# Performance work log

Hardware: AMD Instinct MI355X
Metric: run time of the kernel (lower is better)

## Reference

```python
import jax, jax.numpy as jnp
import numpy as np

B, T, N, D = 32, 50, 100, 4
E = N * (N - 1)
N_IN, N_HID, N_OUT = T * D, 256, 4


def _mlp(x, w1, b1, w2, b2):
    # Linear -> ReLU -> (dropout=0) -> Linear
    return jax.nn.relu(x @ w1 + b1) @ w2 + b2


def setup_inputs() -> dict:
    key = jax.random.key(0)
    ks = jax.random.split(key, 12)
    # fully-connected directed graph, no self loops
    idx = np.array([(i, j) for i in range(N) for j in range(N) if i != j], dtype=np.int64)
    recv, sendr = idx[:, 0], idx[:, 1]
    rec = jnp.asarray(np.eye(N, dtype=np.float32)[recv])    # [E, N]
    send = jnp.asarray(np.eye(N, dtype=np.float32)[sendr])  # [E, N]

    def lin(k, fan_in, fan_out):
        kw, kb = jax.random.split(k)
        w = jax.random.normal(kw, (fan_in, fan_out), jnp.float32) * 0.02
        b = jax.random.normal(kb, (fan_out,), jnp.float32) * 0.02
        return w, b

    x = jax.random.normal(ks[0], (B, T, N, D), jnp.float32)
    w1a, b1a = lin(ks[1], N_IN, N_HID)
    w1b, b1b = lin(ks[2], N_HID, N_HID)
    w2a, b2a = lin(ks[3], 2 * N_HID, N_HID)
    w2b, b2b = lin(ks[4], N_HID, N_HID)
    w3a, b3a = lin(ks[5], N_HID, N_HID)
    w3b, b3b = lin(ks[6], N_HID, N_HID)
    w4a, b4a = lin(ks[7], 3 * N_HID, N_HID)
    w4b, b4b = lin(ks[8], N_HID, N_HID)
    wo, bo = lin(ks[9], N_HID, N_OUT)
    return {"x": x, "rec": rec, "send": send,
            "w1a": w1a, "b1a": b1a, "w1b": w1b, "b1b": b1b,
            "w2a": w2a, "b2a": b2a, "w2b": w2b, "b2b": b2b,
            "w3a": w3a, "b3a": b3a, "w3b": w3b, "b3b": b3b,
            "w4a": w4a, "b4a": b4a, "w4b": w4b, "b4b": b4b,
            "wo": wo, "bo": bo}


def reference(x, rec, send,
              w1a, b1a, w1b, b1b,
              w2a, b2a, w2b, b2b,
              w3a, b3a, w3b, b3b,
              w4a, b4a, w4b, b4b,
              wo, bo):
    # [B, T, N, D] -> [B, N, T*D]
    h = jnp.transpose(x, (0, 2, 1, 3)).reshape(x.shape[0], x.shape[2], -1)
    h = _mlp(h, w1a, b1a, w1b, b1b)                       # [B, N, H]
    # v2e: gather receiver/sender node states to edges
    e = jnp.concatenate([jnp.einsum('en,bnh->beh', rec, h),
                         jnp.einsum('en,bnh->beh', send, h)], axis=2)  # [B, E, 2H]
    e = _mlp(e, w2a, b2a, w2b, b2b)                       # [B, E, H]
    x_skip = e
    # e2v: scatter edges back to nodes, normalize by n_nodes
    v = jnp.einsum('en,beh->bnh', rec, e) / e.shape[-2] * (e.shape[-2] / rec.shape[1])
    v = jnp.einsum('en,beh->bnh', rec, e) / rec.shape[1]  # incoming / incoming.size(1)=N
    v = _mlp(v, w3a, b3a, w3b, b3b)                       # [B, N, H]
    e2 = jnp.concatenate([jnp.einsum('en,bnh->beh', rec, v),
                          jnp.einsum('en,bnh->beh', send, v)], axis=2)  # [B, E, 2H]
    e2 = jnp.concatenate([e2, x_skip], axis=2)            # [B, E, 3H]
    e2 = _mlp(e2, w4a, b4a, w4b, b4b)                     # [B, E, H]
    return e2 @ wo + bo                                   # [B, E, n_out]
```

## Files before the change

### kernel.cpp

```cpp
#include <hip/hip_runtime.h>
#include <hip/hip_bf16.h>
#include <stdint.h>


typedef __attribute__((ext_vector_type(8))) short short8;
typedef __attribute__((ext_vector_type(4))) float float4v;
typedef __attribute__((ext_vector_type(4))) unsigned short ushort4v;
typedef __attribute__((ext_vector_type(4))) unsigned int uint4v;
typedef __attribute__((ext_vector_type(2))) unsigned int uint2v;

__device__ inline float bf2f(unsigned short u) {
    union { unsigned int i; float f; } v; v.i = ((unsigned int)u) << 16; return v.f;
}

#if __has_builtin(__builtin_amdgcn_cvt_pk_bf16_f32)
typedef __attribute__((ext_vector_type(2))) __bf16 bf16x2;
__device__ inline unsigned int f2bf_pk(float a, float b) {
    union { bf16x2 v; unsigned int u; } c;
    c.v = __builtin_amdgcn_cvt_pk_bf16_f32(a, b);
    return c.u;
}
__device__ inline unsigned short f2bf(float f) {
    return (unsigned short)(f2bf_pk(f, f) & 0xFFFFu);
}
#else
__device__ inline unsigned short f2bf(float f) {
    union { float f; unsigned int i; } v; v.f = f;
    unsigned int i = v.i;
    return (unsigned short)((i + 0x7FFFu + ((i >> 16) & 1u)) >> 16);
}
__device__ inline unsigned int f2bf_pk(float a, float b) {
    return (unsigned int)f2bf(a) | ((unsigned int)f2bf(b) << 16);
}
#endif

__global__ __launch_bounds__(256) void prep_kernel(
        const float* __restrict__ x,
        const float* __restrict__ w1a, const float* __restrict__ w1b,
        const float* __restrict__ w2a, const float* __restrict__ w2b,
        const float* __restrict__ w3a, const float* __restrict__ w3b,
        const float* __restrict__ w4a, const float* __restrict__ b4a,
        const float* __restrict__ w4b, const float* __restrict__ b4b,
        const float* __restrict__ wo,  const float* __restrict__ bo,
        const float* __restrict__ b2b,
        unsigned short* __restrict__ Wp1a, unsigned short* __restrict__ Wp1b,
        unsigned short* __restrict__ Wp2r, unsigned short* __restrict__ Wp2s,
        unsigned short* __restrict__ Wp2b, unsigned short* __restrict__ Wp3a,
        unsigned short* __restrict__ Wp3b, unsigned short* __restrict__ Wp4r,
        unsigned short* __restrict__ Wp4s, unsigned short* __restrict__ Wpz,
        unsigned short* __restrict__ Wfp, float* __restrict__ bfv,
        float* __restrict__ b4ap, float* __restrict__ b2bs,
        unsigned short* __restrict__ hin) {
    int bx = blockIdx.x;
    int tid = threadIdx.x;
    if (bx < 2272) {
        const float* W; unsigned short* Wp; int Kin; int b0;
        if      (bx <  224) { W = w1a;             Wp = Wp1a; Kin = 200; b0 = 0;    }
        else if (bx <  480) { W = w1b;             Wp = Wp1b; Kin = 256; b0 = 224;  }
        else if (bx <  736) { W = w2a;             Wp = Wp2r; Kin = 256; b0 = 480;  }
        else if (bx <  992) { W = w2a + 256 * 256; Wp = Wp2s; Kin = 256; b0 = 736;  }
        else if (bx < 1248) { W = w2b;             Wp = Wp2b; Kin = 256; b0 = 992;  }
        else if (bx < 1504) { W = w3a;             Wp = Wp3a; Kin = 256; b0 = 1248; }
        else if (bx < 1760) { W = w3b;             Wp = Wp3b; Kin = 256; b0 = 1504; }
        else if (bx < 2016) { W = w4a;             Wp = Wp4r; Kin = 256; b0 = 1760; }
        else                { W = w4a + 256 * 256; Wp = Wp4s; Kin = 256; b0 = 2016; }
        int idx = (bx - b0) * 256 + tid;
        int k = idx >> 8, n = idx & 255;
        unsigned short v = (k < Kin) ? f2bf(W[k * 256 + n]) : (unsigned short)0;
        Wp[((size_t)(k >> 5) * 256 + n) * 32 + (k & 31)] = v;
    } else if (bx < 2528) {
        int k = bx - 2272, c = tid;
        float s = 0.f;
        for (int t = 0; t < 256; ++t)
            s += w2b[k * 256 + t] * w4a[(size_t)(512 + t) * 256 + c];
        int n = (c & ~31) + (c & 1) * 16 + ((c & 31) >> 1);
        Wpz[((size_t)(k >> 5) * 256 + n) * 32 + (k & 31)] = f2bf(s);
    } else if (bx < 2530) {
        int k = tid;
        if (bx == 2528) {
            float a[4] = {0.f, 0.f, 0.f, 0.f};
            for (int c = 0; c < 256; ++c) {
                float wv = w4b[k * 256 + c];
                #pragma unroll
                for (int o = 0; o < 4; ++o) a[o] += wv * wo[c * 4 + o];
            }
            #pragma unroll
            for (int n = 0; n < 16; ++n)
                Wfp[(size_t)(k >> 5) * 512 + n * 32 + (k & 31)] =
                    (n < 4) ? f2bf(a[n]) : (unsigned short)0;
            if (k < 4) {
                float s = bo[k];
                for (int c = 0; c < 256; ++c) s += b4b[c] * wo[c * 4 + k];
                bfv[k] = s;
            }
        } else {
            float s = b4a[k];
            for (int t = 0; t < 256; ++t)
                s += b2b[t] * w4a[(size_t)(512 + t) * 256 + k];
            b4ap[k] = s;
            b2bs[k] = 0.99f * b2b[k];
        }
    } else {
        int idx = (bx - 2530) * 256 + tid;
        if (idx < 3200 * 224) {
            int row = idx / 224;
            int c = idx - row * 224;
            int b = row / 100, n = row - b * 100;
            unsigned short v = 0;
            if (c < 200) {
                int t = c >> 2, d = c & 3;
                v = f2bf(x[(((size_t)(b * 50 + t)) * 100 + n) * 4 + d]);
            }
            hin[(size_t)row * 224 + c] = v;
        }
    }
}

__global__ __launch_bounds__(512) void node_fusedA_kernel(
        const unsigned short* __restrict__ hin,
        const unsigned short* __restrict__ Wp1a, const float* __restrict__ b1a,
        const unsigned short* __restrict__ Wp1b, const float* __restrict__ b1b,
        const unsigned short* __restrict__ Wp2r, const float* __restrict__ b2a,
        const unsigned short* __restrict__ Wp2s,
        unsigned short* __restrict__ U, unsigned short* __restrict__ Hs) {
    __shared__ __align__(16) unsigned short t1s[16 * 264];
    __shared__ __align__(16) unsigned short hs2[16 * 264];
    const int m0 = blockIdx.x * 16;
    const int tid  = threadIdx.x;
    const int wave = tid >> 6;
    const int lane = tid & 63;
    const int l15  = lane & 15;
    const int quad = lane >> 4;
    const int n0   = wave * 32;
    const int koff = quad * 8;

    {
        float4v acc[2];
        acc[0] = (float4v)(0.0f); acc[1] = (float4v)(0.0f);
        for (int kb = 0; kb < 7; ++kb) {
            short8 af = *(const short8*)(hin + (size_t)(m0 + l15) * 224 + kb * 32 + koff);
            #pragma unroll
            for (int ni = 0; ni < 2; ++ni) {
                short8 bf = *(const short8*)(Wp1a + ((size_t)kb * 256 + n0 + ni * 16 + l15) * 32 + koff);
                acc[ni] = __builtin_amdgcn_mfma_f32_16x16x32_bf16(af, bf, acc[ni], 0, 0, 0);
            }
        }
        #pragma unroll
        for (int ni = 0; ni < 2; ++ni) {
            int col = n0 + ni * 16 + l15;
            float bv = b1a[col];
            #pragma unroll
            for (int r = 0; r < 4; ++r) {
                float v = acc[ni][r] + bv;
                v = v > 0.f ? v : 0.f;
                t1s[(quad * 4 + r) * 264 + col] = f2bf(v);
            }
        }
    }
    __syncthreads();

    {
        float4v acc[2];
        acc[0] = (float4v)(0.0f); acc[1] = (float4v)(0.0f);
        for (int kb = 0; kb < 8; ++kb) {
            short8 af = *(const short8*)(&t1s[l15 * 264 + kb * 32 + koff]);
            #pragma unroll
            for (int ni = 0; ni < 2; ++ni) {
                short8 bf = *(const short8*)(Wp1b + ((size_t)kb * 256 + n0 + ni * 16 + l15) * 32 + koff);
                acc[ni] = __builtin_amdgcn_mfma_f32_16x16x32_bf16(af, bf, acc[ni], 0, 0, 0);
            }
        }
        #pragma unroll
        for (int ni = 0; ni < 2; ++ni) {
            int col = n0 + ni * 16 + l15;
            float bv = b1b[col];
            #pragma unroll
            for (int r = 0; r < 4; ++r)
                hs2[(quad * 4 + r) * 264 + col] = f2bf(acc[ni][r] + bv);
        }
    }
    __syncthreads();

    {
        float4v aU[2], aH[2];
        aU[0] = (float4v)(0.0f); aU[1] = (float4v)(0.0f);
        aH[0] = (float4v)(0.0f); aH[1] = (float4v)(0.0f);
        for (int kb = 0; kb < 8; ++kb) {
            short8 af = *(const short8*)(&hs2[l15 * 264 + kb * 32 + koff]);
            #pragma unroll
            for (int ni = 0; ni < 2; ++ni) {
                short8 bu = *(const short8*)(Wp2r + ((size_t)kb * 256 + n0 + ni * 16 + l15) * 32 + koff);
                short8 bh = *(const short8*)(Wp2s + ((size_t)kb * 256 + n0 + ni * 16 + l15) * 32 + koff);
                aU[ni] = __builtin_amdgcn_mfma_f32_16x16x32_bf16(af, bu, aU[ni], 0, 0, 0);
                aH[ni] = __builtin_amdgcn_mfma_f32_16x16x32_bf16(af, bh, aH[ni], 0, 0, 0);
            }
        }
        #pragma unroll
        for (int ni = 0; ni < 2; ++ni) {
            int col = n0 + ni * 16 + l15;
            float bv = b2a[col];
            #pragma unroll
            for (int r = 0; r < 4; ++r) {
                size_t o = (size_t)(m0 + quad * 4 + r) * 256 + col;
                U[o]  = f2bf(aU[ni][r] + bv);
                Hs[o] = f2bf(aH[ni][r]);
            }
        }
    }
}

__global__ __launch_bounds__(512) void node_fusedC_kernel(
        const unsigned short* __restrict__ U, const unsigned short* __restrict__ Hs,
        const unsigned short* __restrict__ Wp2b, const float* __restrict__ b2bs,
        const unsigned short* __restrict__ Wp3a, const float* __restrict__ b3a,
        const unsigned short* __restrict__ Wp3b, const float* __restrict__ b3b,
        const unsigned short* __restrict__ Wp4r, const float* __restrict__ b4ap,
        const unsigned short* __restrict__ Wp4s,
        unsigned short* __restrict__ C4, unsigned short* __restrict__ Vs) {
    __shared__ __align__(16) unsigned short buf0[16 * 264];
    __shared__ __align__(16) unsigned short buf1[16 * 264];
    const int m0 = blockIdx.x * 16;
    const int tid  = threadIdx.x;
    const int wave = tid >> 6;
    const int lane = tid & 63;
    const int l15  = lane & 15;
    const int quad = lane >> 4;
    const int n0   = wave * 32;
    const int koff = quad * 8;

    {
        const int rl = tid >> 5;
        const int ct = (tid & 31) * 8;
        const int g = m0 + rl;
        const int b = g / 100, i = g - b * 100;
        float u[8], s[8];
        {
            ushort4v u0 = *(const ushort4v*)(U + (size_t)g * 256 + ct);
            ushort4v u1 = *(const ushort4v*)(U + (size_t)g * 256 + ct + 4);
            #pragma unroll
            for (int e = 0; e < 4; ++e) { u[e] = bf2f(u0[e]); u[4 + e] = bf2f(u1[e]); }
            #pragma unroll
            for (int e = 0; e < 8; ++e) s[e] = 0.f;
        }
        const unsigned short* base = Hs + (size_t)b * 100 * 256 + ct;
        #pragma unroll 5
        for (int j = 0; j < 100; ++j) {
            ushort4v h0 = *(const ushort4v*)(base + (size_t)j * 256);
            ushort4v h1 = *(const ushort4v*)(base + (size_t)j * 256 + 4);
            #pragma unroll
            for (int e = 0; e < 4; ++e) {
                float v0 = u[e] + bf2f(h0[e]);     s[e]     += (v0 > 0.f ? v0 : 0.f);
                float v1 = u[4 + e] + bf2f(h1[e]); s[4 + e] += (v1 > 0.f ? v1 : 0.f);
            }
        }
        {
            ushort4v h0 = *(const ushort4v*)(base + (size_t)i * 256);
            ushort4v h1 = *(const ushort4v*)(base + (size_t)i * 256 + 4);
            #pragma unroll
            for (int e = 0; e < 4; ++e) {
                float v0 = u[e] + bf2f(h0[e]);     s[e]     -= (v0 > 0.f ? v0 : 0.f);
                float v1 = u[4 + e] + bf2f(h1[e]); s[4 + e] -= (v1 > 0.f ? v1 : 0.f);
            }
        }
        uint4v d;
        d[0] = f2bf_pk(s[0] * 0.01f, s[1] * 0.01f);
        d[1] = f2bf_pk(s[2] * 0.01f, s[3] * 0.01f);
        d[2] = f2bf_pk(s[4] * 0.01f, s[5] * 0.01f);
        d[3] = f2bf_pk(s[6] * 0.01f, s[7] * 0.01f);
        *(uint4v*)(&buf1[rl * 264 + ct]) = d;
    }
    __syncthreads();

    {
        float4v acc[2];
        acc[0] = (float4v)(0.0f); acc[1] = (float4v)(0.0f);
        for (int kb = 0; kb < 8; ++kb) {
            short8 af = *(const short8*)(&buf1[l15 * 264 + kb * 32 + koff]);
            #pragma unroll
            for (int ni = 0; ni < 2; ++ni) {
                short8 bf = *(const short8*)(Wp2b + ((size_t)kb * 256 + n0 + ni * 16 + l15) * 32 + koff);
                acc[ni] = __builtin_amdgcn_mfma_f32_16x16x32_bf16(af, bf, acc[ni], 0, 0, 0);
            }
        }
        #pragma unroll
        for (int ni = 0; ni < 2; ++ni) {
            int col = n0 + ni * 16 + l15;
            float bv = b2bs[col];
            #pragma unroll
            for (int r = 0; r < 4; ++r)
                buf0[(quad * 4 + r) * 264 + col] = f2bf(acc[ni][r] + bv);
        }
    }
    __syncthreads();

    {
        float4v acc[2];
        acc[0] = (float4v)(0.0f); acc[1] = (float4v)(0.0f);
        for (int kb = 0; kb < 8; ++kb) {
            short8 af = *(const short8*)(&buf0[l15 * 264 + kb * 32 + koff]);
            #pragma unroll
            for (int ni = 0; ni < 2; ++ni) {
                short8 bf = *(const short8*)(Wp3a + ((size_t)kb * 256 + n0 + ni * 16 + l15) * 32 + koff);
                acc[ni] = __builtin_amdgcn_mfma_f32_16x16x32_bf16(af, bf, acc[ni], 0, 0, 0);
            }
        }
        __syncthreads();
        #pragma unroll
        for (int ni = 0; ni < 2; ++ni) {
            int col = n0 + ni * 16 + l15;
            float bv = b3a[col];
            #pragma unroll
            for (int r = 0; r < 4; ++r) {
                float v = acc[ni][r] + bv;
                v = v > 0.f ? v : 0.f;
                buf1[(quad * 4 + r) * 264 + col] = f2bf(v);
            }
        }
    }
    __syncthreads();

    {
        float4v acc[2];
        acc[0] = (float4v)(0.0f); acc[1] = (float4v)(0.0f);
        for (int kb = 0; kb < 8; ++kb) {
            short8 af = *(const short8*)(&buf1[l15 * 264 + kb * 32 + koff]);
            #pragma unroll
            for (int ni = 0; ni < 2; ++ni) {
                short8 bf = *(const short8*)(Wp3b + ((size_t)kb * 256 + n0 + ni * 16 + l15) * 32 + koff);
                acc[ni] = __builtin_amdgcn_mfma_f32_16x16x32_bf16(af, bf, acc[ni], 0, 0, 0);
            }
        }
        __syncthreads();
        #pragma unroll
        for (int ni = 0; ni < 2; ++ni) {
            int col = n0 + ni * 16 + l15;
            float bv = b3b[col];
            #pragma unroll
            for (int r = 0; r < 4; ++r)
                buf0[(quad * 4 + r) * 264 + col] = f2bf(acc[ni][r] + bv);
        }
    }
    __syncthreads();

    {
        float4v aC[2], aV[2];
        aC[0] = (float4v)(0.0f); aC[1] = (float4v)(0.0f);
        aV[0] = (float4v)(0.0f); aV[1] = (float4v)(0.0f);
        for (int kb = 0; kb < 8; ++kb) {
            short8 af = *(const short8*)(&buf0[l15 * 264 + kb * 32 + koff]);
            #pragma unroll
            for (int ni = 0; ni < 2; ++ni) {
                short8 bc = *(const short8*)(Wp4r + ((size_t)kb * 256 + n0 + ni * 16 + l15) * 32 + koff);
                short8 bv = *(const short8*)(Wp4s + ((size_t)kb * 256 + n0 + ni * 16 + l15) * 32 + koff);
                aC[ni] = __builtin_amdgcn_mfma_f32_16x16x32_bf16(af, bc, aC[ni], 0, 0, 0);
                aV[ni] = __builtin_amdgcn_mfma_f32_16x16x32_bf16(af, bv, aV[ni], 0, 0, 0);
            }
        }
        #pragma unroll
        for (int ni = 0; ni < 2; ++ni) {
            int col = n0 + ni * 16 + l15;
            float bv = b4ap[col];
            #pragma unroll
            for (int r = 0; r < 4; ++r) {
                size_t o = (size_t)(m0 + quad * 4 + r) * 256 + col;
                C4[o] = f2bf(aC[ni][r] + bv);
                Vs[o] = f2bf(aV[ni][r]);
            }
        }
    }
}

__global__ __launch_bounds__(512, 6) void edge_phaseB_kernel(
        const unsigned short* __restrict__ Hs, const unsigned short* __restrict__ Vs,
        const unsigned short* __restrict__ U, const unsigned short* __restrict__ C4,
        const unsigned short* __restrict__ Wpz, const unsigned short* __restrict__ Wfp,
        const float* __restrict__ bfv,
        float* __restrict__ out) {
    __shared__ __align__(16) unsigned short t2s[64 * 264];
    const int e0 = blockIdx.x * 64;
    const int b  = blockIdx.y;
    const int nE = (9900 - e0) < 64 ? (9900 - e0) : 64;
    const int nr0 = e0 / 99;
    const int nr1c = (nr0 < 99) ? nr0 + 1 : 99;
    const int br  = (nr0 + 1) * 99 - e0;
    const int bd0 = 100 * nr0 - e0;
    const int bd1 = bd0 + 100;
    const int jb  = e0 - 99 * nr0;
    const unsigned ub100 = (unsigned)(b * 100);
    const int tid  = threadIdx.x;
    const int wave = tid >> 6;
    const int lane = tid & 63;
    const int l15  = lane & 15;
    const int quad = lane >> 4;
    const int n0   = wave * 32;
    const int koff = quad * 8;
    const int cp = n0 + 2 * l15;
    const int rbase = quad * 4;

    unsigned int vsp[16];
    #pragma unroll
    for (int mi = 0; mi < 4; ++mi) {
        #pragma unroll
        for (int r = 0; r < 4; ++r) {
            int row = mi * 16 + rbase + r;
            int jj = jb + row - ((row >= br) ? 100 : 0)
                   + ((row >= bd0) ? 1 : 0) + ((row >= bd1) ? 1 : 0);
            vsp[mi * 4 + r] =
                *(const unsigned int*)(Vs + ((ub100 + (unsigned)jj) << 8) + (unsigned)cp);
        }
    }
    unsigned int c4a = *(const unsigned int*)(C4 + ((ub100 + (unsigned)nr0) << 8) + (unsigned)cp);
    unsigned int c4b = *(const unsigned int*)(C4 + ((ub100 + (unsigned)nr1c) << 8) + (unsigned)cp);
    float c4e0 = bf2f((unsigned short)c4a);
    float c4o0 = bf2f((unsigned short)(c4a >> 16));
    float c4e1 = bf2f((unsigned short)c4b);
    float c4o1 = bf2f((unsigned short)(c4b >> 16));

    {
        const int c = lane * 4;
        ushort4v uva = *(const ushort4v*)(U + ((ub100 + (unsigned)nr0) << 8) + c);
        ushort4v uvb = *(const ushort4v*)(U + ((ub100 + (unsigned)nr1c) << 8) + c);
        float ua0 = bf2f(uva[0]), ua1 = bf2f(uva[1]), ua2 = bf2f(uva[2]), ua3 = bf2f(uva[3]);
        float ub0 = bf2f(uvb[0]), ub1 = bf2f(uvb[1]), ub2 = bf2f(uvb[2]), ub3 = bf2f(uvb[3]);
        for (int r = wave; r < 64; r += 8) {
            int sec = (r >= br) ? 1 : 0;
            int j = jb + r - (sec ? 100 : 0) + ((r >= bd0) ? 1 : 0) + ((r >= bd1) ? 1 : 0);
            ushort4v hv = *(const ushort4v*)(Hs + ((ub100 + (unsigned)j) << 8) + c);
            float t0, t1, t2, t3;
            if (sec) {
                t0 = ub0 + bf2f(hv[0]); t1 = ub1 + bf2f(hv[1]);
                t2 = ub2 + bf2f(hv[2]); t3 = ub3 + bf2f(hv[3]);
            } else {
                t0 = ua0 + bf2f(hv[0]); t1 = ua1 + bf2f(hv[1]);
                t2 = ua2 + bf2f(hv[2]); t3 = ua3 + bf2f(hv[3]);
            }
            t0 = t0 > 0.f ? t0 : 0.f;
            t1 = t1 > 0.f ? t1 : 0.f;
            t2 = t2 > 0.f ? t2 : 0.f;
            t3 = t3 > 0.f ? t3 : 0.f;
            uint2v p;
            p[0] = f2bf_pk(t0, t1);
            p[1] = f2bf_pk(t2, t3);
            *(uint2v*)(&t2s[r * 264 + c]) = p;
        }
    }
    __syncthreads();

    float4v acc[4][2];
    #pragma unroll
    for (int mi = 0; mi < 4; ++mi) {
        acc[mi][0] = (float4v)(0.0f);
        acc[mi][1] = (float4v)(0.0f);
    }

    const unsigned short* wz = Wpz + (((unsigned)(n0 + l15)) << 5) + (unsigned)koff;
    const unsigned short* a0 = t2s + l15 * 264 + koff;
    #pragma unroll 2
    for (int kb = 0; kb < 8; ++kb) {
        short8 bf0 = *(const short8*)(wz);
        short8 bf1 = *(const short8*)(wz + 512);
        #pragma unroll
        for (int mi = 0; mi < 4; ++mi) {
            short8 af = *(const short8*)(a0 + mi * 16 * 264 + kb * 32);
            acc[mi][0] = __builtin_amdgcn_mfma_f32_16x16x32_bf16(af, bf0, acc[mi][0], 0, 0, 0);
            acc[mi][1] = __builtin_amdgcn_mfma_f32_16x16x32_bf16(af, bf1, acc[mi][1], 0, 0, 0);
        }
        wz += 8192;
    }
    __syncthreads();

    #pragma unroll
    for (int mi = 0; mi < 4; ++mi) {
        #pragma unroll
        for (int r = 0; r < 4; ++r) {
            int row = mi * 16 + rbase + r;
            unsigned int vp = vsp[mi * 4 + r];
            float ce = (row >= br) ? c4e1 : c4e0;
            float co = (row >= br) ? c4o1 : c4o0;
            float z0 = bf2f((unsigned short)vp) + ce + acc[mi][0][r];
            float z1 = bf2f((unsigned short)(vp >> 16)) + co + acc[mi][1][r];
            z0 = z0 > 0.f ? z0 : 0.f;
            z1 = z1 > 0.f ? z1 : 0.f;
            *(unsigned int*)(&t2s[row * 264 + cp]) = f2bf_pk(z0, z1);
        }
    }
    __syncthreads();

    if (wave < 4) {
        float4v pacc = (float4v)(0.0f);
        const unsigned short* za0 = t2s + (wave * 16 + l15) * 264 + koff;
        const unsigned short* wf0 = Wfp + (unsigned)(l15 * 32 + koff);
        #pragma unroll
        for (int kb = 0; kb < 8; ++kb) {
            short8 za = *(const short8*)(za0 + kb * 32);
            short8 wb = *(const short8*)(wf0 + kb * 512);
            pacc = __builtin_amdgcn_mfma_f32_16x16x32_bf16(za, wb, pacc, 0, 0, 0);
        }
        if (l15 < 4) {
            float bv = bfv[l15];
            #pragma unroll
            for (int r = 0; r < 4; ++r) {
                int row = wave * 16 + rbase + r;
                if (row < nE)
                    out[(unsigned)((b * 9900 + e0 + row) * 4 + l15)] = pacc[r] + bv;
            }
        }
    }
}

extern "C" void kernel_launch(void* const* d_in, const int* in_sizes, int n_in,
                              void* d_out, int out_size, void* d_ws, size_t ws_size,
                              hipStream_t stream) {
    const float* x   = (const float*)d_in[0];
    const float* w1a = (const float*)d_in[3];
    const float* b1a = (const float*)d_in[4];
    const float* w1b = (const float*)d_in[5];
    const float* b1b = (const float*)d_in[6];
    const float* w2a = (const float*)d_in[7];
    const float* b2a = (const float*)d_in[8];
    const float* w2b = (const float*)d_in[9];
    const float* b2b = (const float*)d_in[10];
    const float* w3a = (const float*)d_in[11];
    const float* b3a = (const float*)d_in[12];
    const float* w3b = (const float*)d_in[13];
    const float* b3b = (const float*)d_in[14];
    const float* w4a = (const float*)d_in[15];
    const float* b4a = (const float*)d_in[16];
    const float* w4b = (const float*)d_in[17];
    const float* b4b = (const float*)d_in[18];
    const float* wo  = (const float*)d_in[19];
    const float* bo  = (const float*)d_in[20];
    float* out = (float*)d_out;
    (void)in_sizes; (void)n_in; (void)out_size; (void)ws_size;

    char* ws = (char*)d_ws;
    size_t off = 0;
    auto alloc = [&](size_t bytes) {
        size_t o = off;
        off = (off + bytes + 255) & ~(size_t)255;
        return o;
    };
    const size_t SLOT_BF = (size_t)3200 * 256 * 2;
    unsigned short* S_U  = (unsigned short*)(ws + alloc(SLOT_BF));
    unsigned short* S_Hs = (unsigned short*)(ws + alloc(SLOT_BF));
    unsigned short* S_Vs = (unsigned short*)(ws + alloc(SLOT_BF));
    unsigned short* S_4  = (unsigned short*)(ws + alloc(SLOT_BF));
    unsigned short* Wp1a = (unsigned short*)(ws + alloc(224 * 256 * 2));
    unsigned short* Wp1b = (unsigned short*)(ws + alloc(256 * 256 * 2));
    unsigned short* Wp2r = (unsigned short*)(ws + alloc(256 * 256 * 2));
    unsigned short* Wp2s = (unsigned short*)(ws + alloc(256 * 256 * 2));
    unsigned short* Wp2b = (unsigned short*)(ws + alloc(256 * 256 * 2));
    unsigned short* Wp3a = (unsigned short*)(ws + alloc(256 * 256 * 2));
    unsigned short* Wp3b = (unsigned short*)(ws + alloc(256 * 256 * 2));
    unsigned short* Wp4r = (unsigned short*)(ws + alloc(256 * 256 * 2));
    unsigned short* Wp4s = (unsigned short*)(ws + alloc(256 * 256 * 2));
    unsigned short* Wpz  = (unsigned short*)(ws + alloc(256 * 256 * 2));
    unsigned short* Wfp  = (unsigned short*)(ws + alloc(8 * 16 * 32 * 2));
    float*          bfv  = (float*)(ws + alloc(4 * 4));
    float*          b4ap = (float*)(ws + alloc(256 * 4));
    float*          b2bs = (float*)(ws + alloc(256 * 4));

    unsigned short* hin = S_4;
    unsigned short* C4  = S_4;

    hipLaunchKernelGGL(prep_kernel, dim3(5330), dim3(256), 0, stream,
                       x, w1a, w1b, w2a, w2b, w3a, w3b, w4a, b4a, w4b, b4b, wo, bo, b2b,
                       Wp1a, Wp1b, Wp2r, Wp2s, Wp2b, Wp3a, Wp3b, Wp4r, Wp4s, Wpz,
                       Wfp, bfv, b4ap, b2bs, hin);
    hipLaunchKernelGGL(node_fusedA_kernel, dim3(200), dim3(512), 0, stream,
                       hin, Wp1a, b1a, Wp1b, b1b, Wp2r, b2a, Wp2s, S_U, S_Hs);
    hipLaunchKernelGGL(node_fusedC_kernel, dim3(200), dim3(512), 0, stream,
                       S_U, S_Hs, Wp2b, b2bs, Wp3a, b3a, Wp3b, b3b, Wp4r, b4ap, Wp4s, C4, S_Vs);
    hipLaunchKernelGGL(edge_phaseB_kernel, dim3(155, 32), dim3(512), 0, stream,
                       S_Hs, S_Vs, S_U, C4, Wpz, Wfp, bfv, out);
}
```

Measured before the change: 238.9 us.

## Make edge phase persistent over four tiles with double-buffered LDS prefetch

The edge kernel now processes four 64-edge tiles per block instead of one, shrinking the grid from 155 to 39 blocks along x. It uses two LDS buffers and prefetches the next tile's Hs/U gathers into registers while the current tile's MFMA loop runs, then stages them into the alternate buffer. The goal is to hide global gather latency and amortise per-block setup. The cost is higher register pressure (launch bounds drop to 4 blocks/SM), double the LDS per block, fewer blocks (1248 total) and an imbalanced last block.

Result: slower. 369.3 us (+54.6%).

```diff
diff --git a/kernel.cpp b/kernel.cpp
--- a/kernel.cpp
+++ b/kernel.cpp
@@ -11,6 +11,12 @@
 
 __device__ inline float bf2f(unsigned short u) {
     union { unsigned int i; float f; } v; v.i = ((unsigned int)u) << 16; return v.f;
+}
+__device__ inline float bf_lo(unsigned int u) {
+    union { unsigned int i; float f; } v; v.i = u << 16; return v.f;
+}
+__device__ inline float bf_hi(unsigned int u) {
+    union { unsigned int i; float f; } v; v.i = u & 0xFFFF0000u; return v.f;
 }
 
 #if __has_builtin(__builtin_amdgcn_cvt_pk_bf16_f32)
@@ -370,22 +376,17 @@
     }
 }
 
-__global__ __launch_bounds__(512, 6) void edge_phaseB_kernel(
+#define TPB_TILES 4
+
+__global__ __launch_bounds__(512, 4) void edge_phaseB_kernel(
         const unsigned short* __restrict__ Hs, const unsigned short* __restrict__ Vs,
         const unsigned short* __restrict__ U, const unsigned short* __restrict__ C4,
         const unsigned short* __restrict__ Wpz, const unsigned short* __restrict__ Wfp,
         const float* __restrict__ bfv,
         float* __restrict__ out) {
-    __shared__ __align__(16) unsigned short t2s[64 * 264];
-    const int e0 = blockIdx.x * 64;
+    __shared__ __align__(16) unsigned short t2s[2][64 * 264];
+    const int tbase = blockIdx.x * TPB_TILES;
     const int b  = blockIdx.y;
-    const int nE = (9900 - e0) < 64 ? (9900 - e0) : 64;
-    const int nr0 = e0 / 99;
-    const int nr1c = (nr0 < 99) ? nr0 + 1 : 99;
-    const int br  = (nr0 + 1) * 99 - e0;
-    const int bd0 = 100 * nr0 - e0;
-    const int bd1 = bd0 + 100;
-    const int jb  = e0 - 99 * nr0;
     const unsigned ub100 = (unsigned)(b * 100);
     const int tid  = threadIdx.x;
     const int wave = tid >> 6;
@@ -394,116 +395,180 @@
     const int quad = lane >> 4;
     const int n0   = wave * 32;
     const int koff = quad * 8;
-    const int cp = n0 + 2 * l15;
+    const int cp   = n0 + 2 * l15;
     const int rbase = quad * 4;
-
-    unsigned int vsp[16];
-    #pragma unroll
-    for (int mi = 0; mi < 4; ++mi) {
-        #pragma unroll
-        for (int r = 0; r < 4; ++r) {
-            int row = mi * 16 + rbase + r;
-            int jj = jb + row - ((row >= br) ? 100 : 0)
-                   + ((row >= bd0) ? 1 : 0) + ((row >= bd1) ? 1 : 0);
-            vsp[mi * 4 + r] =
-                *(const unsigned int*)(Vs + ((ub100 + (unsigned)jj) << 8) + (unsigned)cp);
-        }
-    }
-    unsigned int c4a = *(const unsigned int*)(C4 + ((ub100 + (unsigned)nr0) << 8) + (unsigned)cp);
-    unsigned int c4b = *(const unsigned int*)(C4 + ((ub100 + (unsigned)nr1c) << 8) + (unsigned)cp);
-    float c4e0 = bf2f((unsigned short)c4a);
-    float c4o0 = bf2f((unsigned short)(c4a >> 16));
-    float c4e1 = bf2f((unsigned short)c4b);
-    float c4o1 = bf2f((unsigned short)(c4b >> 16));
-
-    {
-        const int c = lane * 4;
-        ushort4v uva = *(const ushort4v*)(U + ((ub100 + (unsigned)nr0) << 8) + c);
-        ushort4v uvb = *(const ushort4v*)(U + ((ub100 + (unsigned)nr1c) << 8) + c);
-        float ua0 = bf2f(uva[0]), ua1 = bf2f(uva[1]), ua2 = bf2f(uva[2]), ua3 = bf2f(uva[3]);
-        float ub0 = bf2f(uvb[0]), ub1 = bf2f(uvb[1]), ub2 = bf2f(uvb[2]), ub3 = bf2f(uvb[3]);
-        for (int r = wave; r < 64; r += 8) {
-            int sec = (r >= br) ? 1 : 0;
-            int j = jb + r - (sec ? 100 : 0) + ((r >= bd0) ? 1 : 0) + ((r >= bd1) ? 1 : 0);
-            ushort4v hv = *(const ushort4v*)(Hs + ((ub100 + (unsigned)j) << 8) + c);
-            float t0, t1, t2, t3;
-            if (sec) {
-                t0 = ub0 + bf2f(hv[0]); t1 = ub1 + bf2f(hv[1]);
-                t2 = ub2 + bf2f(hv[2]); t3 = ub3 + bf2f(hv[3]);
-            } else {
-                t0 = ua0 + bf2f(hv[0]); t1 = ua1 + bf2f(hv[1]);
-                t2 = ua2 + bf2f(hv[2]); t3 = ua3 + bf2f(hv[3]);
-            }
-            t0 = t0 > 0.f ? t0 : 0.f;
-            t1 = t1 > 0.f ? t1 : 0.f;
-            t2 = t2 > 0.f ? t2 : 0.f;
-            t3 = t3 > 0.f ? t3 : 0.f;
+    const int cst  = lane * 4;
+
+    const int nt = (155 - tbase) < TPB_TILES ? (155 - tbase) : TPB_TILES;
+
+    struct TI { int e0, nE, nr0, nr1c, br, bd0, bd1, jb; };
+    auto tinfo = [](int t) {
+        TI ti; ti.e0 = t * 64;
+        ti.nE   = (9900 - ti.e0) < 64 ? (9900 - ti.e0) : 64;
+        ti.nr0  = ti.e0 / 99;
+        ti.nr1c = (ti.nr0 < 99) ? ti.nr0 + 1 : 99;
+        ti.br   = (ti.nr0 + 1) * 99 - ti.e0;
+        ti.bd0  = 100 * ti.nr0 - ti.e0;
+        ti.bd1  = ti.bd0 + 100;
+        ti.jb   = ti.e0 - 99 * ti.nr0;
+        return ti;
+    };
+    auto jrow = [](const TI& ti, int r) {
+        return ti.jb + r - ((r >= ti.br) ? 100 : 0)
+             + ((r >= ti.bd0) ? 1 : 0) + ((r >= ti.bd1) ? 1 : 0);
+    };
+
+    uint2v hvA[8], hvB[8];
+    uint2v uaA, ubA2, uaB, ubB2;
+    unsigned vspA[16], vspB[16];
+    unsigned c4aA, c4bA, c4aB, c4bB;
+
+    auto issue_hu = [&](int t, uint2v* hv, uint2v& ua, uint2v& ub) {
+        TI ti = tinfo(t);
+        ua = *(const uint2v*)(U + ((ub100 + (unsigned)ti.nr0) << 8) + (unsigned)cst);
+        ub = *(const uint2v*)(U + ((ub100 + (unsigned)ti.nr1c) << 8) + (unsigned)cst);
+        #pragma unroll
+        for (int rr = 0; rr < 8; ++rr) {
+            int r = wave + rr * 8;
+            int j = jrow(ti, r);
+            hv[rr] = *(const uint2v*)(Hs + ((ub100 + (unsigned)j) << 8) + (unsigned)cst);
+        }
+    };
+    auto issue_vc = [&](int t, unsigned* vsp, unsigned& c4a_, unsigned& c4b_) {
+        TI ti = tinfo(t);
+        #pragma unroll
+        for (int mi = 0; mi < 4; ++mi) {
+            #pragma unroll
+            for (int r = 0; r < 4; ++r) {
+                int row = mi * 16 + rbase + r;
+                int jj = jrow(ti, row);
+                vsp[mi * 4 + r] =
+                    *(const unsigned*)(Vs + ((ub100 + (unsigned)jj) << 8) + (unsigned)cp);
+            }
+        }
+        c4a_ = *(const unsigned*)(C4 + ((ub100 + (unsigned)ti.nr0) << 8) + (unsigned)cp);
+        c4b_ = *(const unsigned*)(C4 + ((ub100 + (unsigned)ti.nr1c) << 8) + (unsigned)cp);
+    };
+    auto stage_write = [&](int t, const uint2v* hv, uint2v ua, uint2v ub,
+                           unsigned short* buf) {
+        TI ti = tinfo(t);
+        float ua0 = bf_lo(ua[0]), ua1 = bf_hi(ua[0]), ua2 = bf_lo(ua[1]), ua3 = bf_hi(ua[1]);
+        float ub0 = bf_lo(ub[0]), ub1 = bf_hi(ub[0]), ub2 = bf_lo(ub[1]), ub3 = bf_hi(ub[1]);
+        #pragma unroll
+        for (int rr = 0; rr < 8; ++rr) {
+            int r = wave + rr * 8;
+            float s0, s1, s2, s3;
+            if (r >= ti.br) { s0 = ub0; s1 = ub1; s2 = ub2; s3 = ub3; }
+            else            { s0 = ua0; s1 = ua1; s2 = ua2; s3 = ua3; }
+            float t0 = s0 + bf_lo(hv[rr][0]); t0 = t0 > 0.f ? t0 : 0.f;
+            float t1 = s1 + bf_hi(hv[rr][0]); t1 = t1 > 0.f ? t1 : 0.f;
+            float t2 = s2 + bf_lo(hv[rr][1]); t2 = t2 > 0.f ? t2 : 0.f;
+            float t3 = s3 + bf_hi(hv[rr][1]); t3 = t3 > 0.f ? t3 : 0.f;
             uint2v p;
             p[0] = f2bf_pk(t0, t1);
             p[1] = f2bf_pk(t2, t3);
-            *(uint2v*)(&t2s[r * 264 + c]) = p;
-        }
-    }
+            *(uint2v*)(&buf[r * 264 + cst]) = p;
+        }
+    };
+    auto kloop = [&](const unsigned short* buf, float4v (*acc)[2]) {
+        #pragma unroll
+        for (int mi = 0; mi < 4; ++mi) {
+            acc[mi][0] = (float4v)(0.0f);
+            acc[mi][1] = (float4v)(0.0f);
+        }
+        const unsigned short* wz = Wpz + (((unsigned)(n0 + l15)) << 5) + (unsigned)koff;
+        const unsigned short* a0 = buf + l15 * 264 + koff;
+        #pragma unroll 2
+        for (int kb = 0; kb < 8; ++kb) {
+            short8 bf0 = *(const short8*)(wz);
+            short8 bf1 = *(const short8*)(wz + 512);
+            #pragma unroll
+            for (int mi = 0; mi < 4; ++mi) {
+                short8 af = *(const short8*)(a0 + mi * 16 * 264 + kb * 32);
+                acc[mi][0] = __builtin_amdgcn_mfma_f32_16x16x32_bf16(af, bf0, acc[mi][0], 0, 0, 0);
+                acc[mi][1] = __builtin_amdgcn_mfma_f32_16x16x32_bf16(af, bf1, acc[mi][1], 0, 0, 0);
+            }
+            wz += 8192;
+        }
+    };
+    auto z4w = [&](int t, float4v (*acc)[2], const unsigned* vsp,
+                   unsigned c4a_, unsigned c4b_, unsigned short* buf) {
+        TI ti = tinfo(t);
+        float c4e0 = bf_lo(c4a_), c4o0 = bf_hi(c4a_);
+        float c4e1 = bf_lo(c4b_), c4o1 = bf_hi(c4b_);
+        #pragma unroll
+        for (int mi = 0; mi < 4; ++mi) {
+            #pragma unroll
+            for (int r = 0; r < 4; ++r) {
+                int row = mi * 16 + rbase + r;
+                unsigned vp = vsp[mi * 4 + r];
+                float ce = (row >= ti.br) ? c4e1 : c4e0;
+                float co = (row >= ti.br) ? c4o1 : c4o0;
+                float z0 = bf_lo(vp) + ce + acc[mi][0][r];
+                float z1 = bf_hi(vp) + co + acc[mi][1][r];
+                z0 = z0 > 0.f ? z0 : 0.f;
+                z1 = z1 > 0.f ? z1 : 0.f;
+                *(unsigned*)(&buf[row * 264 + cp]) = f2bf_pk(z0, z1);
+            }
+        }
+    };
+    auto proj = [&](int t, const unsigned short* buf) {
+        TI ti = tinfo(t);
+        if (wave < 4) {
+            float4v pacc = (float4v)(0.0f);
+            const unsigned short* za0 = buf + (wave * 16 + l15) * 264 + koff;
+            const unsigned short* wf0 = Wfp + (unsigned)(l15 * 32 + koff);
+            #pragma unroll
+            for (int kb = 0; kb < 8; ++kb) {
+                short8 za = *(const short8*)(za0 + kb * 32);
+                short8 wb = *(const short8*)(wf0 + kb * 512);
+                pacc = __builtin_amdgcn_mfma_f32_16x16x32_bf16(za, wb, pacc, 0, 0, 0);
+            }
+            if (l15 < 4) {
+                float bv = bfv[l15];
+                #pragma unroll
+                for (int r = 0; r < 4; ++r) {
+                    int row = wave * 16 + rbase + r;
+                    if (row < ti.nE)
+                        out[(unsigned)((b * 9900 + ti.e0 + row) * 4 + l15)] = pacc[r] + bv;
+                }
+            }
+        }
+    };
+
+    issue_hu(tbase, hvA, uaA, ubA2);
+    issue_vc(tbase, vspA, c4aA, c4bA);
+    stage_write(tbase, hvA, uaA, ubA2, t2s[0]);
     __syncthreads();
 
     float4v acc[4][2];
     #pragma unroll
-    for (int mi = 0; mi < 4; ++mi) {
-        acc[mi][0] = (float4v)(0.0f);
-        acc[mi][1] = (float4v)(0.0f);
-    }
-
-    const unsigned short* wz = Wpz + (((unsigned)(n0 + l15)) << 5) + (unsigned)koff;
-    const unsigned short* a0 = t2s + l15 * 264 + koff;
-    #pragma unroll 2
-    for (int kb = 0; kb < 8; ++kb) {
-        short8 bf0 = *(const short8*)(wz);
-        short8 bf1 = *(const short8*)(wz + 512);
-        #pragma unroll
-        for (int mi = 0; mi < 4; ++mi) {
-            short8 af = *(const short8*)(a0 + mi * 16 * 264 + kb * 32);
-            acc[mi][0] = __builtin_amdgcn_mfma_f32_16x16x32_bf16(af, bf0, acc[mi][0], 0, 0, 0);
-            acc[mi][1] = __builtin_amdgcn_mfma_f32_16x16x32_bf16(af, bf1, acc[mi][1], 0, 0, 0);
-        }
-        wz += 8192;
-    }
-    __syncthreads();
-
-    #pragma unroll
-    for (int mi = 0; mi < 4; ++mi) {
-        #pragma unroll
-        for (int r = 0; r < 4; ++r) {
-            int row = mi * 16 + rbase + r;
-            unsigned int vp = vsp[mi * 4 + r];
-            float ce = (row >= br) ? c4e1 : c4e0;
-            float co = (row >= br) ? c4o1 : c4o0;
-            float z0 = bf2f((unsigned short)vp) + ce + acc[mi][0][r];
-            float z1 = bf2f((unsigned short)(vp >> 16)) + co + acc[mi][1][r];
-            z0 = z0 > 0.f ? z0 : 0.f;
-            z1 = z1 > 0.f ? z1 : 0.f;
-            *(unsigned int*)(&t2s[row * 264 + cp]) = f2bf_pk(z0, z1);
-        }
-    }
-    __syncthreads();
-
-    if (wave < 4) {
-        float4v pacc = (float4v)(0.0f);
-        const unsigned short* za0 = t2s + (wave * 16 + l15) * 264 + koff;
-        const unsigned short* wf0 = Wfp + (unsigned)(l15 * 32 + koff);
-        #pragma unroll
-        for (int kb = 0; kb < 8; ++kb) {
-            short8 za = *(const short8*)(za0 + kb * 32);
-            short8 wb = *(const short8*)(wf0 + kb * 512);
-            pacc = __builtin_amdgcn_mfma_f32_16x16x32_bf16(za, wb, pacc, 0, 0, 0);
-        }
-        if (l15 < 4) {
-            float bv = bfv[l15];
-            #pragma unroll
-            for (int r = 0; r < 4; ++r) {
-                int row = wave * 16 + rbase + r;
-                if (row < nE)
-                    out[(unsigned)((b * 9900 + e0 + row) * 4 + l15)] = pacc[r] + bv;
-            }
+    for (int ti = 0; ti < TPB_TILES; ++ti) {
+        if (ti < nt) {
+            const int t = tbase + ti;
+            const bool hasNext = (ti + 1 < nt);
+            unsigned short* bufC = t2s[ti & 1];
+            unsigned short* bufN = t2s[(ti & 1) ^ 1];
+            if (hasNext) {
+                if ((ti & 1) == 0) issue_hu(t + 1, hvB, uaB, ubB2);
+                else               issue_hu(t + 1, hvA, uaA, ubA2);
+            }
+            kloop(bufC, acc);
+            __syncthreads();
+            if ((ti & 1) == 0) z4w(t, acc, vspA, c4aA, c4bA, bufC);
+            else               z4w(t, acc, vspB, c4aB, c4bB, bufC);
+            __syncthreads();
+            proj(t, bufC);
+            if (hasNext) {
+                if ((ti & 1) == 0) {
+                    issue_vc(t + 1, vspB, c4aB, c4bB);
+                    stage_write(t + 1, hvB, uaB, ubB2, bufN);
+                } else {
+                    issue_vc(t + 1, vspA, c4aA, c4bA);
+                    stage_write(t + 1, hvA, uaA, ubA2, bufN);
+                }
+            }
+            __syncthreads();
         }
     }
 }
@@ -571,6 +636,6 @@
                        hin, Wp1a, b1a, Wp1b, b1b, Wp2r, b2a, Wp2s, S_U, S_Hs);
     hipLaunchKernelGGL(node_fusedC_kernel, dim3(200), dim3(512), 0, stream,
                        S_U, S_Hs, Wp2b, b2bs, Wp3a, b3a, Wp3b, b3b, Wp4r, b4ap, Wp4s, C4, S_Vs);
-    hipLaunchKernelGGL(edge_phaseB_kernel, dim3(155, 32), dim3(512), 0, stream,
+    hipLaunchKernelGGL(edge_phaseB_kernel, dim3(39, 32), dim3(512), 0, stream,
                        S_Hs, S_Vs, S_U, C4, Wpz, Wfp, bfv, out);
 }
```
